# Optimization experiments

Hardware: AMD Instinct MI355X
Metric: run time of the kernel (lower is better)

## Reference

```python
import jax, jax.numpy as jnp
import numpy as np

B, S, D, H = 2, 2048, 1024, 16
HD = D // H

def setup_inputs() -> dict:
    key = jax.random.key(0)
    ks = jax.random.split(key, 7)
    s = 1.0 / np.sqrt(D)
    return {
        "x": jax.random.normal(ks[0], (B, S, D), dtype=jnp.float32),
        "Wq": jax.random.uniform(ks[1], (D, D), jnp.float32, -s, s),
        "bq": jax.random.uniform(ks[2], (D,), jnp.float32, -s, s),
        "Wk": jax.random.uniform(ks[3], (D, D), jnp.float32, -s, s),
        "bk": jax.random.uniform(ks[4], (D,), jnp.float32, -s, s),
        "Wv": jax.random.uniform(ks[5], (D, D), jnp.float32, -s, s),
        "bv": jax.random.uniform(ks[6], (D,), jnp.float32, -s, s),
    }

def reference(x, Wq, bq, Wk, bk, Wv, bv):
    b, s, d = x.shape
    def proj(W, bias):
        # [b,s,d] -> [b,H,s,hd]
        y = x @ W + bias
        return y.reshape(b, s, H, HD).transpose(0, 2, 1, 3)
    Q = proj(Wq, bq)
    K = proj(Wk, bk)
    V = proj(Wv, bv)
    # NOTE: original scales by head_dim**0.5 (not sqrt) -> divide by sqrt(HD)
    scores = jnp.einsum("bhqd,bhkd->bhqk", Q, K) / (HD ** 0.5)
    attn = jax.nn.softmax(scores, axis=-1)
    out = jnp.einsum("bhqk,bhkd->bhqd", attn, V)
    out = out.transpose(0, 2, 1, 3).reshape(b, s, d)
    return out + x
```

## Files before the change

kernel.cpp:

```cpp
#include <hip/hip_runtime.h>
#include <stdint.h>

typedef float f32x4 __attribute__((ext_vector_type(4)));
typedef __bf16 bf16x8 __attribute__((ext_vector_type(8)));

union Frag {
    bf16x8 v;
    uint32_t u[4];
    __bf16 e[8];
    uint4 q;
};

constexpr int B_ = 2, S_ = 2048, D_ = 1024, H_ = 16, HD_ = 64;
constexpr int M_ = B_ * S_;

__host__ __device__ constexpr int kperm(int kl) {
    return ((kl & 12) << 1) | ((kl & 16) >> 2) | (kl & 3);
}

typedef const __attribute__((address_space(1))) char gch_t;
typedef __attribute__((address_space(3))) char lch_t;
#define GLD(g, l) __builtin_amdgcn_global_load_lds((gch_t*)(g), (lch_t*)(l), 16, 0, 0)

#define MFMA16(a, b, c) __builtin_amdgcn_mfma_f32_16x16x32_bf16((a), (b), (c), 0, 0, 0)

#define WAIT4 do { asm volatile("s_waitcnt vmcnt(4)" ::: "memory"); \
                   __builtin_amdgcn_sched_barrier(0); } while (0)
#define WAIT2 do { asm volatile("s_waitcnt vmcnt(2)" ::: "memory"); \
                   __builtin_amdgcn_sched_barrier(0); } while (0)
#define WAIT0 do { asm volatile("s_waitcnt vmcnt(0)" ::: "memory"); \
                   __builtin_amdgcn_sched_barrier(0); } while (0)
#define BARR() __builtin_amdgcn_s_barrier()

__global__ void k_cast_x(const float* __restrict__ x, __bf16* __restrict__ xb) {
    int t = blockIdx.x * 256 + threadIdx.x;
    const float4* src = (const float4*)(x + (size_t)t * 32);
    __bf16 buf[32];
#pragma unroll
    for (int j = 0; j < 8; ++j) {
        float4 f = src[j];
        buf[kperm(4 * j + 0)] = (__bf16)f.x;
        buf[kperm(4 * j + 1)] = (__bf16)f.y;
        buf[kperm(4 * j + 2)] = (__bf16)f.z;
        buf[kperm(4 * j + 3)] = (__bf16)f.w;
    }
    uint4* dst = (uint4*)(xb + (size_t)t * 32);
#pragma unroll
    for (int j = 0; j < 4; ++j) dst[j] = ((const uint4*)buf)[j];
}

__global__ void k_prep_w(const float* __restrict__ Wq, const float* __restrict__ Wk,
                         const float* __restrict__ Wv, __bf16* __restrict__ Wt) {
    __shared__ float tile[32][33];
    int p = blockIdx.z;
    const float* W = (p == 0) ? Wq : (p == 1 ? Wk : Wv);
    int n0 = blockIdx.x * 32, k0 = blockIdx.y * 32;
    int tx = threadIdx.x, ty = threadIdx.y;
#pragma unroll
    for (int t = 0; t < 4; ++t)
        tile[ty + 8 * t][tx] = W[(size_t)(k0 + ty + 8 * t) * D_ + n0 + tx];
    __syncthreads();
#pragma unroll
    for (int t = 0; t < 4; ++t)
        Wt[(size_t)(p * D_ + n0 + ty + 8 * t) * D_ + k0 + kperm(tx)] = (__bf16)tile[tx][ty + 8 * t];
}

__global__ __launch_bounds__(512, 4) void k_qkv(
        const __bf16* __restrict__ xb, const __bf16* __restrict__ Wt,
        const float* __restrict__ bq, const float* __restrict__ bk, const float* __restrict__ bv,
        __bf16* __restrict__ Qb, __bf16* __restrict__ Kb, __bf16* __restrict__ Vt) {
    __shared__ __align__(16) char ldsA[2][16384];
    __shared__ __align__(16) char ldsB[2][16384];

    const int tid = threadIdx.x;
    const int lane = tid & 63, wid = tid >> 6;
    const int wr = wid >> 2, wc = wid & 3;
    const int g = lane >> 4, qr = lane & 15, qr7 = qr & 7;
    const int lr = lane >> 3, lp = lane & 7;
    const int c = lp ^ lr;

    int bid = blockIdx.x;
    int xcd = bid & 7, local = bid >> 3;
    int mt = (xcd & 3) * 8 + (local & 7);
    int nt = (xcd >> 2) * 12 + (local >> 3);
    const int m0 = mt * 128, n0 = nt * 128;

    const __bf16* aSrc = xb + (size_t)(m0 + wid * 16 + lr) * D_ + c * 8;
    const __bf16* bSrc = Wt + (size_t)(n0 + wid * 16 + lr) * D_ + c * 8;
    const int dstOff = wid * 16 * 128;

    f32x4 acc[4][2] = {};

    auto STAGE = [&](int buf, int kk) {
        GLD(aSrc + kk,          ldsA[buf] + dstOff);
        GLD(aSrc + kk + 8 * D_, ldsA[buf] + dstOff + 8 * 128);
        GLD(bSrc + kk,          ldsB[buf] + dstOff);
        GLD(bSrc + kk + 8 * D_, ldsB[buf] + dstOff + 8 * 128);
    };
    auto COMPUTE = [&](int buf) {
#pragma unroll
        for (int kc = 0; kc < 2; ++kc) {
            Frag afr[4], bfr[2];
#pragma unroll
            for (int mi = 0; mi < 4; ++mi) {
                int r = wr * 64 + mi * 16 + qr;
                afr[mi].q = *(const uint4*)(ldsA[buf] + r * 128 + (((4 * kc + g) ^ qr7) << 4));
            }
#pragma unroll
            for (int ni = 0; ni < 2; ++ni) {
                int r = wc * 32 + ni * 16 + qr;
                bfr[ni].q = *(const uint4*)(ldsB[buf] + r * 128 + (((4 * kc + g) ^ qr7) << 4));
            }
            __builtin_amdgcn_s_setprio(1);
#pragma unroll
            for (int mi = 0; mi < 4; ++mi)
#pragma unroll
                for (int ni = 0; ni < 2; ++ni)
                    acc[mi][ni] = MFMA16(afr[mi].v, bfr[ni].v, acc[mi][ni]);
            __builtin_amdgcn_s_setprio(0);
        }
    };

    STAGE(0, 0);
    STAGE(1, 64);
    for (int t = 0; t < 12; t += 2) {
        WAIT4; BARR(); COMPUTE(0); BARR(); STAGE(0, (t + 2) * 64);
        WAIT4; BARR(); COMPUTE(1); BARR(); STAGE(1, (t + 3) * 64);
    }
    WAIT4; BARR(); COMPUTE(0); BARR(); STAGE(0, 14 * 64);
    WAIT4; BARR(); COMPUTE(1); BARR(); STAGE(1, 15 * 64);
    WAIT4; BARR(); COMPUTE(0);
    WAIT0; BARR(); COMPUTE(1);

    const int p = n0 >> 10;
    const float* bias = (p == 0) ? bq : (p == 1 ? bk : bv);
#pragma unroll
    for (int ni = 0; ni < 2; ++ni) {
        int n = n0 + wc * 32 + ni * 16 + qr;
        int d = n & 1023;
        float bb = bias[d];
        int h = d >> 6, hd = d & 63;
        int hd_s = (hd & 32) | kperm(hd & 31);
#pragma unroll
        for (int mi = 0; mi < 4; ++mi) {
#pragma unroll
            for (int r = 0; r < 4; ++r) {
                int m = m0 + wr * 64 + mi * 16 + 4 * g + r;
                float vv = acc[mi][ni][r] + bb;
                int b = m >> 11, s = m & 2047;
                if (p == 0) {
                    vv *= 0.18033688f;
                    Qb[((size_t)((b * H_ + h) * S_ + s)) * HD_ + hd_s] = (__bf16)vv;
                } else if (p == 1) {
                    Kb[((size_t)((b * H_ + h) * S_ + s)) * HD_ + hd_s] = (__bf16)vv;
                } else {
                    int s_s = (s & ~31) | kperm(s & 31);
                    Vt[((size_t)((b * H_ + h) * HD_ + hd)) * S_ + s_s] = (__bf16)vv;
                }
            }
        }
    }
}

__global__ __launch_bounds__(512) void k_attn(
        const __bf16* __restrict__ Qb, const __bf16* __restrict__ Kb,
        const __bf16* __restrict__ Vt, const float* __restrict__ x,
        float* __restrict__ out) {
    __shared__ __align__(16) char ldsK[2][8192];
    __shared__ __align__(16) char ldsV[2][8192];

    const int tid = threadIdx.x;
    const int lane = tid & 63, w = tid >> 6;
    const int g = lane >> 4, qr = lane & 15, qr7 = qr & 7;
    const int lr = lane >> 3, lp = lane & 7;
    const int c = lp ^ lr;

    int lid = blockIdx.x;
    int xcd = lid & 7, loc = lid >> 3;
    int bh = xcd * 4 + (loc >> 4);
    int q0 = (loc & 15) * 128;
    const int qrow = q0 + w * 16 + qr;

    Frag qf[2];
    const __bf16* qp = Qb + ((size_t)bh * S_ + qrow) * HD_;
    qf[0].q = *(const uint4*)(qp + g * 8);
    qf[1].q = *(const uint4*)(qp + 32 + g * 8);

    const __bf16* kSrc = Kb + ((size_t)bh * S_ + w * 8 + lr) * HD_ + c * 8;
    const __bf16* vSrc = Vt + ((size_t)bh * HD_ + w * 8 + lr) * S_ + c * 8;
    const int dstOff = w * 8 * 128;

    f32x4 oacc[4] = {};
    f32x4 lacc = {};

    Frag ones;
    ones.u[0] = ones.u[1] = ones.u[2] = ones.u[3] = 0x3f803f80u;

    auto STAGE = [&](int buf, int kv0) {
        GLD(kSrc + (size_t)kv0 * HD_, ldsK[buf] + dstOff);
        GLD(vSrc + kv0,               ldsV[buf] + dstOff);
    };

    auto TILE = [&](int buf) {
        f32x4 sc[4];
        __builtin_amdgcn_s_setprio(1);
#pragma unroll
        for (int kt = 0; kt < 4; ++kt) {
            const char* base = ldsK[buf] + (kt * 16 + qr) * 128;
            Frag k0, k1;
            k0.q = *(const uint4*)(base + ((g ^ qr7) << 4));
            k1.q = *(const uint4*)(base + (((4 + g) ^ qr7) << 4));
            f32x4 z = {};
            z = MFMA16(k0.v, qf[0].v, z);
            z = MFMA16(k1.v, qf[1].v, z);
            sc[kt] = z;
        }
        __builtin_amdgcn_s_setprio(0);

        Frag pa[2];
#pragma unroll
        for (int r = 0; r < 4; ++r) {
            pa[0].e[r]     = (__bf16)__builtin_amdgcn_exp2f(sc[0][r]);
            pa[0].e[4 + r] = (__bf16)__builtin_amdgcn_exp2f(sc[1][r]);
            pa[1].e[r]     = (__bf16)__builtin_amdgcn_exp2f(sc[2][r]);
            pa[1].e[4 + r] = (__bf16)__builtin_amdgcn_exp2f(sc[3][r]);
        }

        __builtin_amdgcn_s_setprio(1);
        lacc = MFMA16(pa[0].v, ones.v, lacc);
        lacc = MFMA16(pa[1].v, ones.v, lacc);

#pragma unroll
        for (int ni = 0; ni < 4; ++ni) {
            const char* base = ldsV[buf] + (ni * 16 + qr) * 128;
            Frag v0, v1;
            v0.q = *(const uint4*)(base + ((g ^ qr7) << 4));
            v1.q = *(const uint4*)(base + (((4 + g) ^ qr7) << 4));
            oacc[ni] = MFMA16(pa[0].v, v0.v, oacc[ni]);
            oacc[ni] = MFMA16(pa[1].v, v1.v, oacc[ni]);
        }
        __builtin_amdgcn_s_setprio(0);
    };

    STAGE(0, 0);
    STAGE(1, 64);
    for (int t = 0; t < 28; t += 2) {
        WAIT2; BARR(); TILE(0); BARR(); STAGE(0, (t + 2) * 64);
        WAIT2; BARR(); TILE(1); BARR(); STAGE(1, (t + 3) * 64);
    }
    WAIT2; BARR(); TILE(0); BARR(); STAGE(0, 30 * 64);
    WAIT2; BARR(); TILE(1); BARR(); STAGE(1, 31 * 64);
    WAIT2; BARR(); TILE(0);
    WAIT0; BARR(); TILE(1);

    float rs[4];
#pragma unroll
    for (int r = 0; r < 4; ++r) rs[r] = 1.0f / lacc[r];

    int b = bh >> 4, h = bh & 15;
#pragma unroll
    for (int ni = 0; ni < 4; ++ni) {
#pragma unroll
        for (int r = 0; r < 4; ++r) {
            int q = q0 + w * 16 + 4 * g + r;
            size_t addr = ((size_t)(b * S_ + q)) * D_ + h * 64 + ni * 16 + qr;
            out[addr] = oacc[ni][r] * rs[r] + x[addr];
        }
    }
}

extern "C" void kernel_launch(void* const* d_in, const int* in_sizes, int n_in,
                              void* d_out, int out_size, void* d_ws, size_t ws_size,
                              hipStream_t stream) {
    const float* x  = (const float*)d_in[0];
    const float* Wq = (const float*)d_in[1];
    const float* bq = (const float*)d_in[2];
    const float* Wk = (const float*)d_in[3];
    const float* bk = (const float*)d_in[4];
    const float* Wv = (const float*)d_in[5];
    const float* bv = (const float*)d_in[6];
    float* out = (float*)d_out;

    char* ws = (char*)d_ws;
    __bf16* xb = (__bf16*)(ws);
    __bf16* Wt = (__bf16*)(ws + 8388608);
    __bf16* Qb = (__bf16*)(ws + 14680064);
    __bf16* Kb = (__bf16*)(ws + 23068672);
    __bf16* Vt = (__bf16*)(ws + 31457280);

    k_cast_x<<<512, 256, 0, stream>>>(x, xb);
    k_prep_w<<<dim3(32, 32, 3), dim3(32, 8), 0, stream>>>(Wq, Wk, Wv, Wt);
    k_qkv<<<768, 512, 0, stream>>>(xb, Wt, bq, bk, bv, Qb, Kb, Vt);
    k_attn<<<512, 512, 0, stream>>>(Qb, Kb, Vt, x, out);
}
```

Measured before the change: 99.49 us.

## Load QKV GEMM weight fragments directly into registers, keeping only activations in LDS

In the QKV projection GEMM, the weight (B) operand no longer goes through LDS. Each wave now loads its own B fragments from global memory straight into double-buffered registers, one k-step ahead, while the activation (A) tile is still staged in LDS. This halves the kernel's shared-memory footprint and removes the B-side LDS reads. Waves that share a column group now fetch the same weight rows twice, and the wait counts are retuned to cover the mixed load streams.

```diff
diff --git a/kernel.cpp b/kernel.cpp
--- a/kernel.cpp
+++ b/kernel.cpp
@@ -24,6 +24,8 @@
 
 #define MFMA16(a, b, c) __builtin_amdgcn_mfma_f32_16x16x32_bf16((a), (b), (c), 0, 0, 0)
 
+#define WAIT6 do { asm volatile("s_waitcnt vmcnt(6)" ::: "memory"); \
+                   __builtin_amdgcn_sched_barrier(0); } while (0)
 #define WAIT4 do { asm volatile("s_waitcnt vmcnt(4)" ::: "memory"); \
                    __builtin_amdgcn_sched_barrier(0); } while (0)
 #define WAIT2 do { asm volatile("s_waitcnt vmcnt(2)" ::: "memory"); \
@@ -70,7 +72,6 @@
         const float* __restrict__ bq, const float* __restrict__ bk, const float* __restrict__ bv,
         __bf16* __restrict__ Qb, __bf16* __restrict__ Kb, __bf16* __restrict__ Vt) {
     __shared__ __align__(16) char ldsA[2][16384];
-    __shared__ __align__(16) char ldsB[2][16384];
 
     const int tid = threadIdx.x;
     const int lane = tid & 63, wid = tid >> 6;
@@ -86,51 +87,76 @@
     const int m0 = mt * 128, n0 = nt * 128;
 
     const __bf16* aSrc = xb + (size_t)(m0 + wid * 16 + lr) * D_ + c * 8;
-    const __bf16* bSrc = Wt + (size_t)(n0 + wid * 16 + lr) * D_ + c * 8;
     const int dstOff = wid * 16 * 128;
 
+    const __bf16* pB0 = Wt + (size_t)(n0 + wc * 32 + qr) * D_ + g * 8;
+    const __bf16* pB1 = pB0 + (size_t)16 * D_;
+
     f32x4 acc[4][2] = {};
+    Frag bX[2][2], bY[2][2];
+    Frag afr[2][4];
 
     auto STAGE = [&](int buf, int kk) {
         GLD(aSrc + kk,          ldsA[buf] + dstOff);
         GLD(aSrc + kk + 8 * D_, ldsA[buf] + dstOff + 8 * 128);
-        GLD(bSrc + kk,          ldsB[buf] + dstOff);
-        GLD(bSrc + kk + 8 * D_, ldsB[buf] + dstOff + 8 * 128);
     };
-    auto COMPUTE = [&](int buf) {
-#pragma unroll
-        for (int kc = 0; kc < 2; ++kc) {
-            Frag afr[4], bfr[2];
-#pragma unroll
-            for (int mi = 0; mi < 4; ++mi) {
-                int r = wr * 64 + mi * 16 + qr;
-                afr[mi].q = *(const uint4*)(ldsA[buf] + r * 128 + (((4 * kc + g) ^ qr7) << 4));
-            }
-#pragma unroll
-            for (int ni = 0; ni < 2; ++ni) {
-                int r = wc * 32 + ni * 16 + qr;
-                bfr[ni].q = *(const uint4*)(ldsB[buf] + r * 128 + (((4 * kc + g) ^ qr7) << 4));
-            }
-            __builtin_amdgcn_s_setprio(1);
-#pragma unroll
-            for (int mi = 0; mi < 4; ++mi)
-#pragma unroll
-                for (int ni = 0; ni < 2; ++ni)
-                    acc[mi][ni] = MFMA16(afr[mi].v, bfr[ni].v, acc[mi][ni]);
-            __builtin_amdgcn_s_setprio(0);
-        }
-    };
+#define LDA(buf_) do { \
+    _Pragma("unroll") \
+    for (int kc = 0; kc < 2; ++kc) \
+    _Pragma("unroll") \
+        for (int mi = 0; mi < 4; ++mi) { \
+            int r = wr * 64 + mi * 16 + qr; \
+            afr[kc][mi].q = *(const uint4*)(ldsA[buf_] + r * 128 + (((4 * kc + g) ^ qr7) << 4)); \
+        } \
+} while (0)
+#define LOADB(dst_, tt_) do { \
+    _Pragma("unroll") \
+    for (int kc = 0; kc < 2; ++kc) { \
+        dst_[kc][0].q = *(const uint4*)(pB0 + (tt_) * 64 + kc * 32); \
+        dst_[kc][1].q = *(const uint4*)(pB1 + (tt_) * 64 + kc * 32); \
+    } \
+} while (0)
+#define MM(bb_) do { \
+    __builtin_amdgcn_s_setprio(1); \
+    _Pragma("unroll") \
+    for (int kc = 0; kc < 2; ++kc) \
+    _Pragma("unroll") \
+        for (int mi = 0; mi < 4; ++mi) \
+    _Pragma("unroll") \
+            for (int ni = 0; ni < 2; ++ni) \
+                acc[mi][ni] = MFMA16(afr[kc][mi].v, bb_[kc][ni].v, acc[mi][ni]); \
+    __builtin_amdgcn_s_setprio(0); \
+} while (0)
 
     STAGE(0, 0);
+    LOADB(bX, 0);
     STAGE(1, 64);
-    for (int t = 0; t < 12; t += 2) {
-        WAIT4; BARR(); COMPUTE(0); BARR(); STAGE(0, (t + 2) * 64);
-        WAIT4; BARR(); COMPUTE(1); BARR(); STAGE(1, (t + 3) * 64);
-    }
-    WAIT4; BARR(); COMPUTE(0); BARR(); STAGE(0, 14 * 64);
-    WAIT4; BARR(); COMPUTE(1); BARR(); STAGE(1, 15 * 64);
-    WAIT4; BARR(); COMPUTE(0);
-    WAIT0; BARR(); COMPUTE(1);
+
+    for (int t = 0; t < 14; t += 2) {
+        WAIT6; BARR();
+        LDA(0);
+        LOADB(bY, t + 1);
+        MM(bX);
+        BARR(); STAGE(0, (t + 2) * 64);
+
+        WAIT6; BARR();
+        LDA(1);
+        LOADB(bX, t + 2);
+        MM(bY);
+        BARR(); STAGE(1, (t + 3) * 64);
+    }
+    WAIT6; BARR();
+    LDA(0);
+    LOADB(bY, 15);
+    MM(bX);
+    BARR();
+    WAIT4; BARR();
+    LDA(1);
+    MM(bY);
+
+#undef LDA
+#undef LOADB
+#undef MM
 
     const int p = n0 >> 10;
     const float* bias = (p == 0) ? bq : (p == 1 ? bk : bv);
```

Result: slower. 127.1 us (+27.7%).
